# Kernel tuning notes

Hardware: AMD Instinct MI355X
Metric: run time of the kernel (lower is better)

Reference implementation:

```python
import jax, jax.numpy as jnp
import numpy as np

# Dimensions (TinyLlama-like)
B, T = 4, 1024
D = 2048          # hidden_size
H, DH = 32, 64    # heads, head_dim
HK = 8            # kv heads (GQA, n_rep = 4)
RQ, RKV = 32, 32  # per-head SVD ranks
RO, RF = 1024, 1024
I = 5632          # intermediate_size
THETA = 10000.0
EPS = 1e-5


def setup_inputs() -> dict:
    key = jax.random.key(0)
    ks = jax.random.split(key, 16)
    p = lambda k, s: jax.random.normal(k, s, jnp.float32) * 0.02
    return {
        "x": jax.random.normal(ks[0], (B, T, D), jnp.float32),
        "ln1_w": jnp.ones((D,), jnp.float32),
        "ln2_w": jnp.ones((D,), jnp.float32),
        "q_Us": p(ks[1], (H, DH, RQ)),  "q_V": p(ks[2], (H, RQ, D)),
        "k_Us": p(ks[3], (HK, DH, RKV)), "k_V": p(ks[4], (HK, RKV, D)),
        "v_Us": p(ks[5], (HK, DH, RKV)), "v_V": p(ks[6], (HK, RKV, D)),
        "o_Us": p(ks[7], (D, RO)),  "o_V": p(ks[8], (RO, H * DH)),
        "g_Us": p(ks[9], (I, RF)),  "g_V": p(ks[10], (RF, D)),
        "u_Us": p(ks[11], (I, RF)), "u_V": p(ks[12], (RF, D)),
        "d_Us": p(ks[13], (D, RF)), "d_V": p(ks[14], (RF, I)),
    }


def _rms(x, w):
    return x * jax.lax.rsqrt(jnp.mean(x * x, axis=-1, keepdims=True) + EPS) * w


def _rope_cos_sin(t_len, dh, dtype):
    half = dh // 2
    inv_freq = 1.0 / (THETA ** (jnp.arange(half, dtype=jnp.float32) / half))
    ang = jnp.arange(t_len, dtype=jnp.float32)[:, None] * inv_freq[None, :]  # [T, half]
    return jnp.cos(ang).astype(dtype), jnp.sin(ang).astype(dtype)


def _apply_rope(x, cos, sin):
    # x: [B,h,T,Dh], LLaMA half-split rotation
    half = x.shape[-1] // 2
    x1, x2 = x[..., :half], x[..., half:]
    c = cos[None, None]  # [1,1,T,half]
    s = sin[None, None]
    return jnp.concatenate([x1 * c - x2 * s, x2 * c + x1 * s], axis=-1)


def reference(x, ln1_w, ln2_w, q_Us, q_V, k_Us, k_V, v_Us, v_V,
              o_Us, o_V, g_Us, g_V, u_Us, u_V, d_Us, d_V):
    b, t, d = x.shape
    h1 = _rms(x, ln1_w)

    # per-head low-rank projections: y_h = x @ V_h^T @ Us_h^T
    q = jnp.einsum('bhtr,hdr->bhtd', jnp.einsum('btD,hrD->bhtr', h1, q_V), q_Us)  # [B,H,T,Dh]
    k = jnp.einsum('bhtr,hdr->bhtd', jnp.einsum('btD,hrD->bhtr', h1, k_V), k_Us)  # [B,Hk,T,Dh]
    v = jnp.einsum('bhtr,hdr->bhtd', jnp.einsum('btD,hrD->bhtr', h1, v_V), v_Us)

    cos, sin = _rope_cos_sin(t, DH, x.dtype)
    q = _apply_rope(q, cos, sin)
    k = _apply_rope(k, cos, sin)

    n_rep = H // HK
    k = jnp.repeat(k, n_rep, axis=1)  # _repeat_kv
    v = jnp.repeat(v, n_rep, axis=1)

    scale = 1.0 / np.sqrt(DH)
    scores = jnp.einsum('bhtd,bhsd->bhts', q, k) * scale
    causal = jnp.tril(jnp.ones((t, t), bool))
    scores = jnp.where(causal[None, None], scores, jnp.finfo(scores.dtype).min)
    attn = jax.nn.softmax(scores, axis=-1)
    ctx = jnp.einsum('bhts,bhsd->bhtd', attn, v)
    ctx = ctx.transpose(0, 2, 1, 3).reshape(b, t, H * DH)

    # low-rank output proj: o = ctx @ o_V^T @ o_Us^T
    attn_out = jnp.einsum('btr,Dr->btD', jnp.einsum('btk,rk->btr', ctx, o_V), o_Us)
    x = x + attn_out

    # SwiGLU MLP with low-rank factors
    h2 = _rms(x, ln2_w)
    g = jnp.einsum('btr,ir->bti', jnp.einsum('btD,rD->btr', h2, g_V), g_Us)
    u = jnp.einsum('btr,ir->bti', jnp.einsum('btD,rD->btr', h2, u_V), u_Us)
    ff = jax.nn.silu(g) * u
    down = jnp.einsum('btr,Dr->btD', jnp.einsum('bti,ri->btr', ff, d_V), d_Us)
    return x + down
```

## Files before the change

kernel.cpp:

```cpp
#include <hip/hip_runtime.h>
#include <math.h>

typedef unsigned short u16;
typedef unsigned int u32;
typedef __bf16 bf16x8 __attribute__((ext_vector_type(8)));
typedef float f32x4 __attribute__((ext_vector_type(4)));

__device__ __forceinline__ float bf2f(u16 u) {
  union { u32 i; float f; } x; x.i = ((u32)u) << 16; return x.f;
}
__device__ __forceinline__ u16 f2bf(float f) {
  union { float f; u32 i; } x; x.f = f;
  return (u16)((x.i + 0x7fffu + ((x.i >> 16) & 1u)) >> 16);
}

#define GLDS16(gp, lp)                                                        \
  __builtin_amdgcn_global_load_lds(                                           \
      (const __attribute__((address_space(1))) u32*)(gp),                     \
      (__attribute__((address_space(3))) u32*)(lp), 16, 0, 0)

__global__ void detect_k(const u16* __restrict__ w, int* __restrict__ flag) {
  if (threadIdx.x == 0 && blockIdx.x == 0)
    *flag = (w[0] == 0x0000u && w[1] == 0x3F80u) ? 1 : 0;
}

struct CvtArgs {
  const void* src[17];
  u32 dstOff[17];
  u32 blkOff[18];
};

__global__ __launch_bounds__(256) void cvt_all(CvtArgs a, u16* __restrict__ dstB,
                                               const int* __restrict__ flag) {
  int seg = 0;
  const int bx = blockIdx.x;
#pragma unroll 1
  while (bx >= (int)a.blkOff[seg + 1]) seg++;
  const long local = ((long)(bx - a.blkOff[seg]) * 256 + threadIdx.x) * 8;
  u16* dst = dstB + a.dstOff[seg] + local;
  if (*flag) {
    const float* s = (const float*)a.src[seg] + local;
    float4 va = *(const float4*)(s);
    float4 vb = *(const float4*)(s + 4);
    uint4 o; u16* op = (u16*)&o;
    op[0] = f2bf(va.x); op[1] = f2bf(va.y); op[2] = f2bf(va.z); op[3] = f2bf(va.w);
    op[4] = f2bf(vb.x); op[5] = f2bf(vb.y); op[6] = f2bf(vb.z); op[7] = f2bf(vb.w);
    *(uint4*)dst = o;
  } else {
    *(uint4*)dst = *(const uint4*)((const u16*)a.src[seg] + local);
  }
}

__global__ __launch_bounds__(256) void rms_k(const u16* __restrict__ x,
                                             const u16* __restrict__ w,
                                             u16* __restrict__ out) {
  const long row = blockIdx.x;
  const u16* xr = x + row * 2048;
  u16* orow = out + row * 2048;
  const int tid = threadIdx.x;
  const int base = tid * 8;
  uint4 u = *(const uint4*)(xr + base);
  const u16* us = (const u16*)&u;
  float v[8];
  float ss = 0.f;
#pragma unroll
  for (int i = 0; i < 8; i++) { v[i] = bf2f(us[i]); ss += v[i] * v[i]; }
#pragma unroll
  for (int off = 32; off > 0; off >>= 1) ss += __shfl_xor(ss, off);
  __shared__ float red[4];
  if ((tid & 63) == 0) red[tid >> 6] = ss;
  __syncthreads();
  float total = red[0] + red[1] + red[2] + red[3];
  float inv = rsqrtf(total * (1.0f / 2048.0f) + 1e-5f);
  uint4 wv = *(const uint4*)(w + base);
  const u16* wp = (const u16*)&wv;
  uint4 o;
  u16* op = (u16*)&o;
#pragma unroll
  for (int i = 0; i < 8; i++) op[i] = f2bf(v[i] * inv * bf2f(wp[i]));
  *(uint4*)(orow + base) = o;
}

template <int EPI>
__global__ __launch_bounds__(256, 2) void gemm_bt(const u16* __restrict__ A,
                                                  const u16* __restrict__ B,
                                                  void* Cv,
                                                  const u16* R,
                                                  const int* flagp,
                                                  int N, int K, int lda) {
  __shared__ u16 As[128 * 32];
  __shared__ u16 Bs[128 * 32];
  const int m0 = blockIdx.y * 128;
  const int n0 = blockIdx.x * 128;
  const int tid = threadIdx.x;
  const int wave = tid >> 6;
  const int lane = tid & 63;
  const int wr = (wave >> 1) * 64;
  const int wc = (wave & 1) * 64;
  const int l16 = lane & 15;
  const int quad = lane >> 4;
  u16* C = (u16*)Cv;
  float* Cf = (float*)Cv;
  bool f32o = false;
  if (EPI == 3) f32o = (*flagp != 0);

  f32x4 acc[4][4];
#pragma unroll
  for (int i = 0; i < 4; i++)
#pragma unroll
    for (int j = 0; j < 4; j++) acc[i][j] = (f32x4){0.f, 0.f, 0.f, 0.f};

  const int srow = wave * 16 + (lane >> 2);
  const int scol = (lane & 3) * 8;
  const u16* Ag = A + (long)(m0 + srow) * lda + scol;
  const u16* Bg = B + (long)(n0 + srow) * K + scol;
  const long astep = (long)64 * lda;
  const long bstep = (long)64 * K;
  u16* Asw = &As[wave * 16 * 32];
  u16* Bsw = &Bs[wave * 16 * 32];

  for (int k0 = 0; k0 < K; k0 += 32) {
    GLDS16(Ag + k0, Asw);
    GLDS16(Ag + astep + k0, Asw + 64 * 32);
    GLDS16(Bg + k0, Bsw);
    GLDS16(Bg + bstep + k0, Bsw + 64 * 32);
    __syncthreads();
    bf16x8 af[4], bfr[4];
#pragma unroll
    for (int t = 0; t < 4; t++) {
      af[t]  = *(const bf16x8*)(&As[(wr + t * 16 + l16) * 32 + quad * 8]);
      bfr[t] = *(const bf16x8*)(&Bs[(wc + t * 16 + l16) * 32 + quad * 8]);
    }
#pragma unroll
    for (int i = 0; i < 4; i++)
#pragma unroll
      for (int j = 0; j < 4; j++)
        acc[i][j] = __builtin_amdgcn_mfma_f32_16x16x32_bf16(af[i], bfr[j], acc[i][j], 0, 0, 0);
    __syncthreads();
  }

#pragma unroll
  for (int i = 0; i < 4; i++) {
#pragma unroll
    for (int j = 0; j < 4; j++) {
#pragma unroll
      for (int r = 0; r < 4; r++) {
        const int row = m0 + wr + i * 16 + quad * 4 + r;
        const int col = n0 + wc + j * 16 + l16;
        const long idx = (long)row * N + col;
        float v = acc[i][j][r];
        if (EPI == 1 || EPI == 3) v += bf2f(R[idx]);
        if (EPI == 2) {
          float g = bf2f(R[idx]);
          v *= g / (1.f + __expf(-g));
        }
        if (EPI == 3) {
          if (f32o) Cf[idx] = v; else C[idx] = f2bf(v);
        } else {
          C[idx] = f2bf(v);
        }
      }
    }
  }
}

__global__ __launch_bounds__(256) void expand_k(const u16* __restrict__ rbuf,
                                                int rstride,
                                                const u16* __restrict__ Us,
                                                u16* __restrict__ out,
                                                int nheads, int doRope) {
  const int tok = blockIdx.x;
  const int wave = threadIdx.x >> 6;
  const int d = threadIdx.x & 63;
  const int h = blockIdx.y * 4 + wave;
  const int b = tok >> 10;
  const int t = tok & 1023;
  const u16* up = Us + ((long)h * 64 + d) * 32;
  const u16* rp = rbuf + (long)tok * rstride + h * 32;
  float s = 0.f;
#pragma unroll
  for (int c = 0; c < 4; c++) {
    uint4 uu = *(const uint4*)(up + c * 8);
    uint4 rr = *(const uint4*)(rp + c * 8);
    const u16* u8p = (const u16*)&uu;
    const u16* r8p = (const u16*)&rr;
#pragma unroll
    for (int i = 0; i < 8; i++) s += bf2f(u8p[i]) * bf2f(r8p[i]);
  }
  if (doRope) {
    const int j = d & 31;
    float inv = powf(10000.0f, -(float)j * (1.0f / 32.0f));
    float ang = (float)t * inv;
    float sn, cs;
    sincosf(ang, &sn, &cs);
    float partner = __shfl_xor(s, 32);
    s = (d < 32) ? (s * cs - partner * sn) : (s * cs + partner * sn);
  }
  out[(((long)(b * nheads + h)) * 1024 + t) * 64 + d] = f2bf(s);
}

#define ATS 72

__global__ __launch_bounds__(256, 2) void attn_mfma(const u16* __restrict__ q,
                                                    const u16* __restrict__ k,
                                                    const u16* __restrict__ v,
                                                    u16* __restrict__ ctx) {
  __shared__ u16 Ks[64 * ATS];
  __shared__ u16 Vts[64 * ATS];
  __shared__ u16 Plds[4][16 * ATS];
  const int h = blockIdx.y;
  const int b = blockIdx.z;
  const int kh = h >> 2;
  const int qbase = blockIdx.x * 64;
  const int tid = threadIdx.x;
  const int wave = tid >> 6;
  const int lane = tid & 63;
  const int l16 = lane & 15;
  const int quad = lane >> 4;
  const int qrow0w = qbase + wave * 16;

  const u16* qb = q + ((long)(b * 32 + h) * 1024) * 64;
  const u16* kb = k + ((long)(b * 8 + kh) * 1024) * 64;
  const u16* vb = v + ((long)(b * 8 + kh) * 1024) * 64;

  bf16x8 qf[2];
  {
    const u16* qp = qb + (long)(qrow0w + l16) * 64 + quad * 8;
    qf[0] = *(const bf16x8*)(qp);
    qf[1] = *(const bf16x8*)(qp + 32);
  }

  float m[4], l[4];
  f32x4 oacc[4];
#pragma unroll
  for (int r = 0; r < 4; r++) { m[r] = -1e30f; l[r] = 0.f; }
#pragma unroll
  for (int j = 0; j < 4; j++) oacc[j] = (f32x4){0.f, 0.f, 0.f, 0.f};

  const int srow = tid >> 2;
  const int sc0 = (tid & 3) * 16;
  const int rot = (4 * (tid & 3) + (tid >> 2)) & 15;

  for (int s0 = 0; s0 <= qbase; s0 += 64) {
    __syncthreads();
    {
      const u16* kp = kb + (long)(s0 + srow) * 64 + sc0;
      uint4 k0v = *(const uint4*)(kp);
      uint4 k1v = *(const uint4*)(kp + 8);
      *(uint4*)(&Ks[srow * ATS + sc0]) = k0v;
      *(uint4*)(&Ks[srow * ATS + sc0 + 8]) = k1v;
      union { uint4 u[2]; u16 e[16]; } vv;
      const u16* vp = vb + (long)(s0 + srow) * 64 + sc0;
      vv.u[0] = *(const uint4*)(vp);
      vv.u[1] = *(const uint4*)(vp + 8);
#pragma unroll
      for (int ii = 0; ii < 16; ii++) {
        const int i = (ii + rot) & 15;
        Vts[(sc0 + i) * ATS + srow] = vv.e[i];
      }
    }
    __syncthreads();

    f32x4 s[4];
#pragma unroll
    for (int t = 0; t < 4; t++) {
      s[t] = (f32x4){0.f, 0.f, 0.f, 0.f};
      const u16* kr = &Ks[(t * 16 + l16) * ATS + quad * 8];
      bf16x8 b0 = *(const bf16x8*)(kr);
      bf16x8 b1 = *(const bf16x8*)(kr + 32);
      s[t] = __builtin_amdgcn_mfma_f32_16x16x32_bf16(qf[0], b0, s[t], 0, 0, 0);
      s[t] = __builtin_amdgcn_mfma_f32_16x16x32_bf16(qf[1], b1, s[t], 0, 0, 0);
    }
#pragma unroll
    for (int t = 0; t < 4; t++) s[t] *= 0.125f;
    if (s0 == qbase) {
#pragma unroll
      for (int t = 0; t < 4; t++)
#pragma unroll
        for (int r = 0; r < 4; r++)
          if (s0 + t * 16 + l16 > qrow0w + quad * 4 + r) s[t][r] = -1e30f;
    }

    float p[4][4];
#pragma unroll
    for (int r = 0; r < 4; r++) {
      float mx = fmaxf(fmaxf(s[0][r], s[1][r]), fmaxf(s[2][r], s[3][r]));
#pragma unroll
      for (int off = 1; off < 16; off <<= 1) mx = fmaxf(mx, __shfl_xor(mx, off));
      const float mnew = fmaxf(m[r], mx);
      const float alpha = __expf(m[r] - mnew);
      float ps = 0.f;
#pragma unroll
      for (int t = 0; t < 4; t++) { p[t][r] = __expf(s[t][r] - mnew); ps += p[t][r]; }
#pragma unroll
      for (int off = 1; off < 16; off <<= 1) ps += __shfl_xor(ps, off);
      l[r] = l[r] * alpha + ps;
      m[r] = mnew;
#pragma unroll
      for (int j = 0; j < 4; j++) oacc[j][r] *= alpha;
    }

    u16* pw = &Plds[wave][0];
#pragma unroll
    for (int t = 0; t < 4; t++)
#pragma unroll
      for (int r = 0; r < 4; r++)
        pw[(quad * 4 + r) * ATS + t * 16 + l16] = f2bf(p[t][r]);
    bf16x8 pf0 = *(const bf16x8*)(&pw[l16 * ATS + quad * 8]);
    bf16x8 pf1 = *(const bf16x8*)(&pw[l16 * ATS + 32 + quad * 8]);

#pragma unroll
    for (int j = 0; j < 4; j++) {
      const u16* vr = &Vts[(j * 16 + l16) * ATS + quad * 8];
      bf16x8 v0 = *(const bf16x8*)(vr);
      bf16x8 v1 = *(const bf16x8*)(vr + 32);
      oacc[j] = __builtin_amdgcn_mfma_f32_16x16x32_bf16(pf0, v0, oacc[j], 0, 0, 0);
      oacc[j] = __builtin_amdgcn_mfma_f32_16x16x32_bf16(pf1, v1, oacc[j], 0, 0, 0);
    }
  }

#pragma unroll
  for (int r = 0; r < 4; r++) {
    const int row = qrow0w + quad * 4 + r;
    const float inv = 1.f / l[r];
#pragma unroll
    for (int j = 0; j < 4; j++)
      ctx[(((long)(b * 1024 + row)) * 32 + h) * 64 + j * 16 + l16] =
          f2bf(oacc[j][r] * inv);
  }
}

extern "C" void kernel_launch(void* const* d_in, const int* in_sizes, int n_in,
                              void* d_out, int out_size, void* d_ws, size_t ws_size,
                              hipStream_t stream) {
  char* ws = (char*)d_ws;
  u16* cb = (u16*)ws;
  u16* cx    = cb + 0;
  u16* cln1  = cb + 8388608;
  u16* cln2  = cb + 8390656;
  u16* cqUs  = cb + 8392704;
  u16* ckUs  = cb + 8458240;
  u16* cvUs  = cb + 8474624;
  u16* cqkvV = cb + 8491008;
  u16* coUs  = cb + 11636736;
  u16* coV   = cb + 13733888;
  u16* cguV  = cb + 15831040;
  u16* cgUs  = cb + 20025344;
  u16* cuUs  = cb + 25792512;
  u16* cdUs  = cb + 31559680;
  u16* cdV   = cb + 33656832;

  char* P = ws + 78848000;
  u16* h1   = (u16*)(P + 0);
  u16* qkvr = (u16*)(P + 16777216);
  u16* qbuf = (u16*)(P + 33554432);
  u16* kbuf = (u16*)(P + 50331648);
  u16* vbuf = (u16*)(P + 54525952);
  u16* ctx  = (u16*)(P + 58720256);
  u16* orr  = (u16*)(P + 75497472);
  u16* xmid = (u16*)(P + 83886080);
  u16* h2   = (u16*)(P + 0);
  u16* gur  = (u16*)(P + 16777216);
  u16* gbuf = (u16*)(P + 33554432);
  u16* dr   = (u16*)(P + 16777216);
  int* flag = (int*)(ws + 179511296);

  const dim3 blk(256);
  detect_k<<<1, 64, 0, stream>>>((const u16*)d_in[1], flag);

  CvtArgs ca;
  const u32 dOff[17] = {0u, 8388608u, 8390656u, 8392704u, 8491008u, 8458240u,
                        10588160u, 8474624u, 11112448u, 11636736u, 13733888u,
                        20025344u, 15831040u, 25792512u, 17928192u, 31559680u,
                        33656832u};
  const u32 nblk[17] = {4096u, 1u, 1u, 32u, 1024u, 8u, 256u, 8u, 256u, 1024u,
                        1024u, 2816u, 1024u, 2816u, 1024u, 1024u, 2816u};
  u32 cum = 0;
  for (int i = 0; i < 17; i++) {
    ca.src[i] = d_in[i];
    ca.dstOff[i] = dOff[i];
    ca.blkOff[i] = cum;
    cum += nblk[i];
  }
  ca.blkOff[17] = cum;
  cvt_all<<<cum, blk, 0, stream>>>(ca, cb, flag);

  rms_k<<<4096, blk, 0, stream>>>(cx, cln1, h1);
  gemm_bt<0><<<dim3(12, 32), blk, 0, stream>>>(h1, cqkvV, qkvr, nullptr, nullptr, 1536, 2048, 2048);
  expand_k<<<dim3(4096, 8), blk, 0, stream>>>(qkvr, 1536, cqUs, qbuf, 32, 1);
  expand_k<<<dim3(4096, 2), blk, 0, stream>>>(qkvr + 1024, 1536, ckUs, kbuf, 8, 1);
  expand_k<<<dim3(4096, 2), blk, 0, stream>>>(qkvr + 1280, 1536, cvUs, vbuf, 8, 0);
  attn_mfma<<<dim3(16, 32, 4), blk, 0, stream>>>(qbuf, kbuf, vbuf, ctx);
  gemm_bt<0><<<dim3(8, 32), blk, 0, stream>>>(ctx, coV, orr, nullptr, nullptr, 1024, 2048, 2048);
  gemm_bt<1><<<dim3(16, 32), blk, 0, stream>>>(orr, coUs, xmid, cx, nullptr, 2048, 1024, 1024);
  rms_k<<<4096, blk, 0, stream>>>(xmid, cln2, h2);
  gemm_bt<0><<<dim3(16, 32), blk, 0, stream>>>(h2, cguV, gur, nullptr, nullptr, 2048, 2048, 2048);
  gemm_bt<0><<<dim3(44, 32), blk, 0, stream>>>(gur, cgUs, gbuf, nullptr, nullptr, 5632, 1024, 2048);
  gemm_bt<2><<<dim3(44, 32), blk, 0, stream>>>(gur + 1024, cuUs, gbuf, gbuf, nullptr, 5632, 1024, 2048);
  gemm_bt<0><<<dim3(8, 32), blk, 0, stream>>>(gbuf, cdV, dr, nullptr, nullptr, 1024, 5632, 5632);
  gemm_bt<3><<<dim3(16, 32), blk, 0, stream>>>(dr, cdUs, d_out, xmid, flag, 2048, 1024, 1024);
}
```

Before: 933.0 us.

## Split-K small-N GEMMs, pair causal attention blocks, pre-transpose V

The under-occupied GEMMs (QKV, o_V and d_V projections, which launch only 256-384 blocks) are split along K into two launches whose partial results are summed by a new combine kernel. The split is meant to raise GPU occupancy, at the cost of extra bf16 partial buffers, an additional rounding step and more launches. Attention now pairs a low and a high causal query tile in each block so every block does equal work, halving the grid. V is pre-transposed by a separate kernel so the attention loop stores vector rows instead of scalar transposed writes to LDS.

```diff
diff --git a/kernel.cpp b/kernel.cpp
--- a/kernel.cpp
+++ b/kernel.cpp
@@ -87,7 +87,7 @@
                                                   void* Cv,
                                                   const u16* R,
                                                   const int* flagp,
-                                                  int N, int K, int lda) {
+                                                  int N, int Klen, int lda, int ldb) {
   __shared__ u16 As[128 * 32];
   __shared__ u16 Bs[128 * 32];
   const int m0 = blockIdx.y * 128;
@@ -113,13 +113,13 @@
   const int srow = wave * 16 + (lane >> 2);
   const int scol = (lane & 3) * 8;
   const u16* Ag = A + (long)(m0 + srow) * lda + scol;
-  const u16* Bg = B + (long)(n0 + srow) * K + scol;
+  const u16* Bg = B + (long)(n0 + srow) * ldb + scol;
   const long astep = (long)64 * lda;
-  const long bstep = (long)64 * K;
+  const long bstep = (long)64 * ldb;
   u16* Asw = &As[wave * 16 * 32];
   u16* Bsw = &Bs[wave * 16 * 32];
 
-  for (int k0 = 0; k0 < K; k0 += 32) {
+  for (int k0 = 0; k0 < Klen; k0 += 32) {
     GLDS16(Ag + k0, Asw);
     GLDS16(Ag + astep + k0, Asw + 64 * 32);
     GLDS16(Bg + k0, Bsw);
@@ -164,6 +164,20 @@
   }
 }
 
+__global__ __launch_bounds__(256) void combine2(const u16* __restrict__ a,
+                                                const u16* __restrict__ b,
+                                                u16* __restrict__ o) {
+  const long i = ((long)blockIdx.x * 256 + threadIdx.x) * 8;
+  uint4 ua = *(const uint4*)(a + i);
+  uint4 ub = *(const uint4*)(b + i);
+  const u16* pa = (const u16*)&ua;
+  const u16* pb = (const u16*)&ub;
+  uint4 uo; u16* po = (u16*)&uo;
+#pragma unroll
+  for (int j = 0; j < 8; j++) po[j] = f2bf(bf2f(pa[j]) + bf2f(pb[j]));
+  *(uint4*)(o + i) = uo;
+}
+
 __global__ __launch_bounds__(256) void expand_k(const u16* __restrict__ rbuf,
                                                 int rstride,
                                                 const u16* __restrict__ Us,
@@ -199,68 +213,73 @@
   out[(((long)(b * nheads + h)) * 1024 + t) * 64 + d] = f2bf(s);
 }
 
+__global__ __launch_bounds__(256) void vT_k(const u16* __restrict__ vbuf,
+                                            u16* __restrict__ vT) {
+  __shared__ u16 tile[64][72];
+  const int b = blockIdx.z, kh = blockIdx.y;
+  const int t0 = blockIdx.x * 64;
+  const int tid = threadIdx.x;
+  const int r = tid >> 2;
+  const int c = (tid & 3) * 16;
+  const u16* src = vbuf + ((long)(b * 8 + kh) * 1024 + t0 + r) * 64 + c;
+  *(uint4*)&tile[r][c] = *(const uint4*)src;
+  *(uint4*)&tile[r][c + 8] = *(const uint4*)(src + 8);
+  __syncthreads();
+  u16 tmp[16];
+#pragma unroll
+  for (int i = 0; i < 16; i++) tmp[i] = tile[c + i][r];
+  u16* dst = vT + ((long)(b * 8 + kh) * 64 + r) * 1024 + t0 + c;
+  *(uint4*)dst = *(uint4*)&tmp[0];
+  *(uint4*)(dst + 8) = *(uint4*)&tmp[8];
+}
+
 #define ATS 72
 
 __global__ __launch_bounds__(256, 2) void attn_mfma(const u16* __restrict__ q,
                                                     const u16* __restrict__ k,
-                                                    const u16* __restrict__ v,
+                                                    const u16* __restrict__ vT,
                                                     u16* __restrict__ ctx) {
   __shared__ u16 Ks[64 * ATS];
   __shared__ u16 Vts[64 * ATS];
   __shared__ u16 Plds[4][16 * ATS];
+  const int bx = blockIdx.x;
   const int h = blockIdx.y;
   const int b = blockIdx.z;
   const int kh = h >> 2;
-  const int qbase = blockIdx.x * 64;
+  const int qlo = bx * 64;
+  const int qhi = (15 - bx) * 64;
   const int tid = threadIdx.x;
   const int wave = tid >> 6;
   const int lane = tid & 63;
   const int l16 = lane & 15;
   const int quad = lane >> 4;
-  const int qrow0w = qbase + wave * 16;
 
   const u16* qb = q + ((long)(b * 32 + h) * 1024) * 64;
   const u16* kb = k + ((long)(b * 8 + kh) * 1024) * 64;
-  const u16* vb = v + ((long)(b * 8 + kh) * 1024) * 64;
-
-  bf16x8 qf[2];
+  const u16* vb = vT + ((long)(b * 8 + kh) * 64) * 1024;
+
+  bf16x8 qfl[2], qfh[2];
   {
-    const u16* qp = qb + (long)(qrow0w + l16) * 64 + quad * 8;
-    qf[0] = *(const bf16x8*)(qp);
-    qf[1] = *(const bf16x8*)(qp + 32);
-  }
-
-  float m[4], l[4];
-  f32x4 oacc[4];
-#pragma unroll
-  for (int r = 0; r < 4; r++) { m[r] = -1e30f; l[r] = 0.f; }
-#pragma unroll
-  for (int j = 0; j < 4; j++) oacc[j] = (f32x4){0.f, 0.f, 0.f, 0.f};
+    const u16* qp = qb + (long)(qlo + wave * 16 + l16) * 64 + quad * 8;
+    qfl[0] = *(const bf16x8*)(qp);
+    qfl[1] = *(const bf16x8*)(qp + 32);
+    qp = qb + (long)(qhi + wave * 16 + l16) * 64 + quad * 8;
+    qfh[0] = *(const bf16x8*)(qp);
+    qfh[1] = *(const bf16x8*)(qp + 32);
+  }
+
+  float ml[4], ll[4], mh[4], lh[4];
+  f32x4 ol[4], oh[4];
+#pragma unroll
+  for (int r = 0; r < 4; r++) { ml[r] = -1e30f; ll[r] = 0.f; mh[r] = -1e30f; lh[r] = 0.f; }
+#pragma unroll
+  for (int j = 0; j < 4; j++) { ol[j] = (f32x4){0.f, 0.f, 0.f, 0.f}; oh[j] = ol[j]; }
 
   const int srow = tid >> 2;
   const int sc0 = (tid & 3) * 16;
-  const int rot = (4 * (tid & 3) + (tid >> 2)) & 15;
-
-  for (int s0 = 0; s0 <= qbase; s0 += 64) {
-    __syncthreads();
-    {
-      const u16* kp = kb + (long)(s0 + srow) * 64 + sc0;
-      uint4 k0v = *(const uint4*)(kp);
-      uint4 k1v = *(const uint4*)(kp + 8);
-      *(uint4*)(&Ks[srow * ATS + sc0]) = k0v;
-      *(uint4*)(&Ks[srow * ATS + sc0 + 8]) = k1v;
-      union { uint4 u[2]; u16 e[16]; } vv;
-      const u16* vp = vb + (long)(s0 + srow) * 64 + sc0;
-      vv.u[0] = *(const uint4*)(vp);
-      vv.u[1] = *(const uint4*)(vp + 8);
-#pragma unroll
-      for (int ii = 0; ii < 16; ii++) {
-        const int i = (ii + rot) & 15;
-        Vts[(sc0 + i) * ATS + srow] = vv.e[i];
-      }
-    }
-    __syncthreads();
-
+  int s0 = 0;
+
+  auto process = [&](const bf16x8* qf, float* m, float* l, f32x4* oacc, int qtb) {
     f32x4 s[4];
 #pragma unroll
     for (int t = 0; t < 4; t++) {
@@ -273,14 +292,13 @@
     }
 #pragma unroll
     for (int t = 0; t < 4; t++) s[t] *= 0.125f;
-    if (s0 == qbase) {
+    if (s0 == qtb) {
 #pragma unroll
       for (int t = 0; t < 4; t++)
 #pragma unroll
         for (int r = 0; r < 4; r++)
-          if (s0 + t * 16 + l16 > qrow0w + quad * 4 + r) s[t][r] = -1e30f;
-    }
-
+          if (s0 + t * 16 + l16 > qtb + wave * 16 + quad * 4 + r) s[t][r] = -1e30f;
+    }
     float p[4][4];
 #pragma unroll
     for (int r = 0; r < 4; r++) {
@@ -299,7 +317,6 @@
 #pragma unroll
       for (int j = 0; j < 4; j++) oacc[j][r] *= alpha;
     }
-
     u16* pw = &Plds[wave][0];
 #pragma unroll
     for (int t = 0; t < 4; t++)
@@ -308,7 +325,6 @@
         pw[(quad * 4 + r) * ATS + t * 16 + l16] = f2bf(p[t][r]);
     bf16x8 pf0 = *(const bf16x8*)(&pw[l16 * ATS + quad * 8]);
     bf16x8 pf1 = *(const bf16x8*)(&pw[l16 * ATS + 32 + quad * 8]);
-
 #pragma unroll
     for (int j = 0; j < 4; j++) {
       const u16* vr = &Vts[(j * 16 + l16) * ATS + quad * 8];
@@ -317,16 +333,34 @@
       oacc[j] = __builtin_amdgcn_mfma_f32_16x16x32_bf16(pf0, v0, oacc[j], 0, 0, 0);
       oacc[j] = __builtin_amdgcn_mfma_f32_16x16x32_bf16(pf1, v1, oacc[j], 0, 0, 0);
     }
+  };
+
+  for (s0 = 0; s0 <= qhi; s0 += 64) {
+    __syncthreads();
+    {
+      const u16* kp = kb + (long)(s0 + srow) * 64 + sc0;
+      *(uint4*)&Ks[srow * ATS + sc0] = *(const uint4*)kp;
+      *(uint4*)&Ks[srow * ATS + sc0 + 8] = *(const uint4*)(kp + 8);
+      const u16* vp = vb + (long)srow * 1024 + s0 + sc0;
+      *(uint4*)&Vts[srow * ATS + sc0] = *(const uint4*)vp;
+      *(uint4*)&Vts[srow * ATS + sc0 + 8] = *(const uint4*)(vp + 8);
+    }
+    __syncthreads();
+    process(qfh, mh, lh, oh, qhi);
+    if (s0 <= qlo) process(qfl, ml, ll, ol, qlo);
   }
 
 #pragma unroll
   for (int r = 0; r < 4; r++) {
-    const int row = qrow0w + quad * 4 + r;
-    const float inv = 1.f / l[r];
-#pragma unroll
-    for (int j = 0; j < 4; j++)
-      ctx[(((long)(b * 1024 + row)) * 32 + h) * 64 + j * 16 + l16] =
-          f2bf(oacc[j][r] * inv);
+    const int rowl = qlo + wave * 16 + quad * 4 + r;
+    const int rowh = qhi + wave * 16 + quad * 4 + r;
+    const float il = 1.f / ll[r];
+    const float ih = 1.f / lh[r];
+#pragma unroll
+    for (int j = 0; j < 4; j++) {
+      ctx[(((long)(b * 1024 + rowl)) * 32 + h) * 64 + j * 16 + l16] = f2bf(ol[j][r] * il);
+      ctx[(((long)(b * 1024 + rowh)) * 32 + h) * 64 + j * 16 + l16] = f2bf(oh[j][r] * ih);
+    }
   }
 }
 
@@ -351,19 +385,26 @@
   u16* cdV   = cb + 33656832;
 
   char* P = ws + 78848000;
-  u16* h1   = (u16*)(P + 0);
-  u16* qkvr = (u16*)(P + 16777216);
-  u16* qbuf = (u16*)(P + 33554432);
-  u16* kbuf = (u16*)(P + 50331648);
-  u16* vbuf = (u16*)(P + 54525952);
-  u16* ctx  = (u16*)(P + 58720256);
-  u16* orr  = (u16*)(P + 75497472);
-  u16* xmid = (u16*)(P + 83886080);
-  u16* h2   = (u16*)(P + 0);
-  u16* gur  = (u16*)(P + 16777216);
-  u16* gbuf = (u16*)(P + 33554432);
-  u16* dr   = (u16*)(P + 16777216);
-  int* flag = (int*)(ws + 179511296);
+  u16* h1    = (u16*)(P + 0);
+  u16* qkvr  = (u16*)(P + 16777216);
+  u16* qp0   = (u16*)(P + 33554432);
+  u16* qp1   = (u16*)(P + 46137344);
+  u16* qbuf  = (u16*)(P + 33554432);
+  u16* kbuf  = (u16*)(P + 50331648);
+  u16* vbuf  = (u16*)(P + 54525952);
+  u16* ctx   = (u16*)(P + 58720256);
+  u16* vbufT = (u16*)(P + 75497472);
+  u16* orr   = (u16*)(P + 75497472);
+  u16* xmid  = (u16*)(P + 83886080);
+  u16* op0   = (u16*)(P + 0);
+  u16* op1   = (u16*)(P + 8388608);
+  u16* h2    = (u16*)(P + 0);
+  u16* gur   = (u16*)(P + 16777216);
+  u16* gbuf  = (u16*)(P + 33554432);
+  u16* dp0   = (u16*)(P + 0);
+  u16* dp1   = (u16*)(P + 8388608);
+  u16* dr    = (u16*)(P + 16777216);
+  int* flag  = (int*)(ws + 179511296);
 
   const dim3 blk(256);
   detect_k<<<1, 64, 0, stream>>>((const u16*)d_in[1], flag);
@@ -386,17 +427,24 @@
   cvt_all<<<cum, blk, 0, stream>>>(ca, cb, flag);
 
   rms_k<<<4096, blk, 0, stream>>>(cx, cln1, h1);
-  gemm_bt<0><<<dim3(12, 32), blk, 0, stream>>>(h1, cqkvV, qkvr, nullptr, nullptr, 1536, 2048, 2048);
+  gemm_bt<0><<<dim3(12, 32), blk, 0, stream>>>(h1, cqkvV, qp0, nullptr, nullptr, 1536, 1024, 2048, 2048);
+  gemm_bt<0><<<dim3(12, 32), blk, 0, stream>>>(h1 + 1024, cqkvV + 1024, qp1, nullptr, nullptr, 1536, 1024, 2048, 2048);
+  combine2<<<3072, blk, 0, stream>>>(qp0, qp1, qkvr);
   expand_k<<<dim3(4096, 8), blk, 0, stream>>>(qkvr, 1536, cqUs, qbuf, 32, 1);
   expand_k<<<dim3(4096, 2), blk, 0, stream>>>(qkvr + 1024, 1536, ckUs, kbuf, 8, 1);
   expand_k<<<dim3(4096, 2), blk, 0, stream>>>(qkvr + 1280, 1536, cvUs, vbuf, 8, 0);
-  attn_mfma<<<dim3(16, 32, 4), blk, 0, stream>>>(qbuf, kbuf, vbuf, ctx);
-  gemm_bt<0><<<dim3(8, 32), blk, 0, stream>>>(ctx, coV, orr, nullptr, nullptr, 1024, 2048, 2048);
-  gemm_bt<1><<<dim3(16, 32), blk, 0, stream>>>(orr, coUs, xmid, cx, nullptr, 2048, 1024, 1024);
+  vT_k<<<dim3(16, 8, 4), blk, 0, stream>>>(vbuf, vbufT);
+  attn_mfma<<<dim3(8, 32, 4), blk, 0, stream>>>(qbuf, kbuf, vbufT, ctx);
+  gemm_bt<0><<<dim3(8, 32), blk, 0, stream>>>(ctx, coV, op0, nullptr, nullptr, 1024, 1024, 2048, 2048);
+  gemm_bt<0><<<dim3(8, 32), blk, 0, stream>>>(ctx + 1024, coV + 1024, op1, nullptr, nullptr, 1024, 1024, 2048, 2048);
+  combine2<<<2048, blk, 0, stream>>>(op0, op1, orr);
+  gemm_bt<1><<<dim3(16, 32), blk, 0, stream>>>(orr, coUs, xmid, cx, nullptr, 2048, 1024, 1024, 1024);
   rms_k<<<4096, blk, 0, stream>>>(xmid, cln2, h2);
-  gemm_bt<0><<<dim3(16, 32), blk, 0, stream>>>(h2, cguV, gur, nullptr, nullptr, 2048, 2048, 2048);
-  gemm_bt<0><<<dim3(44, 32), blk, 0, stream>>>(gur, cgUs, gbuf, nullptr, nullptr, 5632, 1024, 2048);
-  gemm_bt<2><<<dim3(44, 32), blk, 0, stream>>>(gur + 1024, cuUs, gbuf, gbuf, nullptr, 5632, 1024, 2048);
-  gemm_bt<0><<<dim3(8, 32), blk, 0, stream>>>(gbuf, cdV, dr, nullptr, nullptr, 1024, 5632, 5632);
-  gemm_bt<3><<<dim3(16, 32), blk, 0, stream>>>(dr, cdUs, d_out, xmid, flag, 2048, 1024, 1024);
-}
+  gemm_bt<0><<<dim3(16, 32), blk, 0, stream>>>(h2, cguV, gur, nullptr, nullptr, 2048, 2048, 2048, 2048);
+  gemm_bt<0><<<dim3(44, 32), blk, 0, stream>>>(gur, cgUs, gbuf, nullptr, nullptr, 5632, 1024, 2048, 1024);
+  gemm_bt<2><<<dim3(44, 32), blk, 0, stream>>>(gur + 1024, cuUs, gbuf, gbuf, nullptr, 5632, 1024, 2048, 1024);
+  gemm_bt<0><<<dim3(8, 32), blk, 0, stream>>>(gbuf, cdV, dp0, nullptr, nullptr, 1024, 2816, 5632, 5632);
+  gemm_bt<0><<<dim3(8, 32), blk, 0, stream>>>(gbuf + 2816, cdV + 2816, dp1, nullptr, nullptr, 1024, 2816, 5632, 5632);
+  combine2<<<2048, blk, 0, stream>>>(dp0, dp1, dr);
+  gemm_bt<3><<<dim3(16, 32), blk, 0, stream>>>(dr, cdUs, d_out, xmid, flag, 2048, 1024, 1024, 1024);
+}
```

New measurement: 887.1 us. 4.9% less time.
